# Kernel optimization log

Hardware: AMD Instinct MI355X
Metric: run time of the kernel (lower is better)

The kernel has to match this reference:

```python
import jax, jax.numpy as jnp
import numpy as np

N_NODES = 50000
IN_DIM = 256
OUT_DIM = 128
NUM_HEADS = 2
N_EDGES = 800000


def setup_inputs() -> dict:
    key = jax.random.key(0)
    k1, k2, k3, k4, k5 = jax.random.split(key, 5)
    x = jax.random.normal(k1, (N_NODES, IN_DIM), dtype=jnp.float32)
    edge_index = jax.random.randint(k2, (2, N_EDGES), 0, N_NODES, dtype=jnp.int64)
    # Linear(in_dim, out_dim*num_heads): store weight as [in_dim, out_dim*num_heads]
    fan = IN_DIM + OUT_DIM * NUM_HEADS
    W_w = jax.random.uniform(k3, (IN_DIM, OUT_DIM * NUM_HEADS), dtype=jnp.float32,
                             minval=-np.sqrt(6.0 / fan), maxval=np.sqrt(6.0 / fan))
    W_b = jnp.zeros((OUT_DIM * NUM_HEADS,), dtype=jnp.float32)
    # attention vector a: [2*out_dim], xavier uniform over (1, 2*out_dim)
    fa = 1 + 2 * OUT_DIM
    a = jax.random.uniform(k4, (2 * OUT_DIM,), dtype=jnp.float32,
                           minval=-np.sqrt(6.0 / fa), maxval=np.sqrt(6.0 / fa))
    return {"x": x, "edge_index": edge_index, "W_w": W_w, "W_b": W_b, "a": a}


def _gat_forward(x, edge_index, W_w, W_b, a):
    N = x.shape[0]
    H, D = NUM_HEADS, OUT_DIM
    Wh = (x @ W_w + W_b).reshape(N, H, D)  # [N, H, D]
    src, dst = edge_index[0], edge_index[1]
    a_src, a_dst = a[:D], a[D:]
    # per-node partial scores, then gather -> avoids [E, 2D] concat
    s = jnp.einsum('nhd,d->nh', Wh, a_src)  # [N, H]
    t = jnp.einsum('nhd,d->nh', Wh, a_dst)  # [N, H]
    e = jax.nn.leaky_relu(s[src] + t[dst], negative_slope=0.2)  # [E, H]
    # segment softmax over edges grouped by src node
    m = jax.ops.segment_max(e, src, num_segments=N)  # [N, H], -inf for empty
    ex = jnp.exp(e - m[src])
    denom = jax.ops.segment_sum(ex, src, num_segments=N)  # [N, H]
    alpha = ex / denom[src]  # [E, H]
    # weighted aggregation of destination features into source nodes
    agg = jax.ops.segment_sum(alpha[:, :, None] * Wh[dst], src, num_segments=N)  # [N, H, D]
    deg = jax.ops.segment_sum(jnp.ones_like(src, dtype=Wh.dtype), src, num_segments=N)  # [N]
    h_prime = jnp.where(deg[:, None, None] > 0, agg, Wh)
    return h_prime.reshape(N, H * D)


def reference(x, edge_index, W_w, W_b, a):
    return _gat_forward(x, edge_index, W_w, W_b, a)
```

## Files before the change

### kernel.cpp

```cpp
#include <hip/hip_runtime.h>
#include <hip/hip_bf16.h>
#include <math.h>

#define N_NODES 50000
#define IN_DIM 256
#define OUT_DIM 128
#define NUM_HEADS 2
#define N_EDGES 800000
#define F (OUT_DIM*NUM_HEADS)
#define SCAN_B 1024
#define N_SB ((N_NODES + SCAN_B - 1) / SCAN_B)
#define LDSP 264
#define CAP 128
#define N_COPIES 8
#define NBLK_H (N_EDGES / 256)

typedef __bf16 bf16;
typedef __bf16 bf16x8 __attribute__((ext_vector_type(8)));
typedef float  f32x4  __attribute__((ext_vector_type(4)));
typedef unsigned short u16x8 __attribute__((ext_vector_type(8)));

__global__ void k_transpose(const float* __restrict__ W, bf16* __restrict__ Wt,
                            int* __restrict__ deg8) {
    int k = blockIdx.x;
    int n = threadIdx.x;
    Wt[(size_t)n*IN_DIM + k] = (bf16)W[(size_t)k*F + n];
    int id = blockIdx.x * F + threadIdx.x;
    for (int i = id; i < N_COPIES * N_NODES; i += IN_DIM * F)
        deg8[i] = 0;
}

__global__ __launch_bounds__(256) void k_hist(const int* __restrict__ src,
                                              int* __restrict__ deg8,
                                              unsigned char* __restrict__ rank,
                                              int* __restrict__ xcdtab) {
    unsigned xcc;
    asm volatile("s_getreg_b32 %0, hwreg(HW_REG_XCC_ID, 0, 4)" : "=s"(xcc));
    xcc &= (N_COPIES - 1);
    if (threadIdx.x == 0) xcdtab[blockIdx.x] = (int)xcc;
    int e = blockIdx.x * 256 + threadIdx.x;
    int s = src[e];
    int r = __hip_atomic_fetch_add(&deg8[(size_t)xcc * N_NODES + s], 1,
                                   __ATOMIC_RELAXED, __HIP_MEMORY_SCOPE_WORKGROUP);
    rank[e] = (unsigned char)r;
}

__global__ __launch_bounds__(256, 2) void k_gemm(const float* __restrict__ X,
                                              const bf16* __restrict__ Wt,
                                              const float* __restrict__ Wb,
                                              const float* __restrict__ Av,
                                              bf16* __restrict__ Wh,
                                              float* __restrict__ s_arr,
                                              float* __restrict__ t_arr) {
    __shared__ bf16 As[64 * LDSP];
    __shared__ float sS[2][64], sT[2][64];
    int t = threadIdx.x;
    int wave = t >> 6, lane = t & 63;
    int quad = lane >> 4, l16 = lane & 15;
    int row0 = blockIdx.x * 64;
    int col0 = wave * 64;
    int h = wave >> 1;

    int rr = t >> 5;
    int cc = (t & 31) * 8;
    f32x4 slo[8], shi[8];
    #pragma unroll
    for (int i = 0; i < 8; ++i) {
        int r = row0 + 8*i + rr;
        r = (r < N_NODES) ? r : (N_NODES - 1);
        const float* p = X + (size_t)r * IN_DIM + cc;
        slo[i] = *(const f32x4*)p;
        shi[i] = *(const f32x4*)(p + 4);
    }

    bf16x8 bfrag[4][8];
    #pragma unroll
    for (int ni = 0; ni < 4; ++ni)
        #pragma unroll
        for (int ks = 0; ks < 8; ++ks)
            bfrag[ni][ks] = *(const bf16x8*)(Wt + (size_t)(col0 + ni*16 + l16)*IN_DIM
                                                + ks*32 + quad*8);

    #pragma unroll
    for (int i = 0; i < 8; ++i) {
        bf16x8 pk;
        #pragma unroll
        for (int q = 0; q < 4; ++q) {
            pk[q]   = (bf16)slo[i][q];
            pk[q+4] = (bf16)shi[i][q];
        }
        *(bf16x8*)(As + (8*i + rr) * LDSP + cc) = pk;
    }
    if (t < 128) { sS[t >> 6][t & 63] = 0.f; sT[t >> 6][t & 63] = 0.f; }
    __syncthreads();

    f32x4 acc[4][4] = {};
    #pragma unroll
    for (int ks = 0; ks < 8; ++ks) {
        int kb = ks * 32;
        bf16x8 afrag[4];
        #pragma unroll
        for (int mi = 0; mi < 4; ++mi)
            afrag[mi] = *(const bf16x8*)(As + (mi*16 + l16)*LDSP + kb + quad*8);

        #pragma unroll
        for (int mi = 0; mi < 4; ++mi)
            #pragma unroll
            for (int ni = 0; ni < 4; ++ni)
                acc[mi][ni] = __builtin_amdgcn_mfma_f32_16x16x32_bf16(
                                  afrag[mi], bfrag[ni][ks], acc[mi][ni], 0, 0, 0);
    }

    float bias_l[4], as_l[4], at_l[4];
    #pragma unroll
    for (int ni = 0; ni < 4; ++ni) {
        int c = col0 + ni*16 + l16;
        int d = c & (OUT_DIM - 1);
        bias_l[ni] = Wb[c];
        as_l[ni]   = Av[d];
        at_l[ni]   = Av[OUT_DIM + d];
    }

    #pragma unroll
    for (int mi = 0; mi < 4; ++mi) {
        #pragma unroll
        for (int reg = 0; reg < 4; ++reg) {
            int rl = mi*16 + quad*4 + reg;
            float ps = 0.f, pt = 0.f;
            #pragma unroll
            for (int ni = 0; ni < 4; ++ni) {
                float val = acc[mi][ni][reg] + bias_l[ni];
                ps += val * as_l[ni];
                pt += val * at_l[ni];
            }
            #pragma unroll
            for (int m = 8; m >= 1; m >>= 1) {
                ps += __shfl_xor(ps, m);
                pt += __shfl_xor(pt, m);
            }
            if ((lane & 15) == 0) {
                atomicAdd(&sS[h][rl], ps);
                atomicAdd(&sT[h][rl], pt);
            }
        }
    }

    __syncthreads();
    #pragma unroll
    for (int mi = 0; mi < 4; ++mi)
        #pragma unroll
        for (int ni = 0; ni < 4; ++ni) {
            int ccc = col0 + ni*16 + l16;
            #pragma unroll
            for (int reg = 0; reg < 4; ++reg) {
                int rl = mi*16 + quad*4 + reg;
                As[rl*LDSP + ccc] = (bf16)(acc[mi][ni][reg] + bias_l[ni]);
            }
        }
    __syncthreads();

    #pragma unroll
    for (int i = 0; i < 8; ++i) {
        int idx = i * 2048 + t * 8;
        int row = idx >> 8;
        int ccw = idx & 255;
        bf16x8 v = *(const bf16x8*)(As + row*LDSP + ccw);
        int grow = row0 + row;
        if (grow < N_NODES)
            *(bf16x8*)(Wh + (size_t)grow*F + ccw) = v;
    }

    if (t < 128) {
        int hh = t >> 6, rl = t & 63;
        int n = row0 + rl;
        if (n < N_NODES) {
            s_arr[n*2 + hh] = sS[hh][rl];
            t_arr[n*2 + hh] = sT[hh][rl];
        }
    }
}

__global__ __launch_bounds__(SCAN_B) void k_scan_local(const int* __restrict__ deg8,
                                                       int* __restrict__ excl,
                                                       int* __restrict__ bsum,
                                                       unsigned short* __restrict__ prefix8) {
    __shared__ int lds[SCAN_B];
    int t = threadIdx.x;
    int i = blockIdx.x * SCAN_B + t;
    int v = 0;
    if (i < N_NODES) {
        u16x8 pf;
        int run = 0;
        #pragma unroll
        for (int c = 0; c < N_COPIES; ++c) {
            pf[c] = (unsigned short)run;
            run += deg8[(size_t)c * N_NODES + i];
        }
        v = run;
        *(u16x8*)(prefix8 + (size_t)i * 8) = pf;
    }
    lds[t] = v;
    __syncthreads();
    for (int off = 1; off < SCAN_B; off <<= 1) {
        int u = (t >= off) ? lds[t - off] : 0;
        __syncthreads();
        lds[t] += u;
        __syncthreads();
    }
    if (i < N_NODES) excl[i] = lds[t] - v;
    if (t == SCAN_B - 1) bsum[blockIdx.x] = lds[t];
}

__global__ __launch_bounds__(256) void k_scan_final(const int* __restrict__ excl,
                                                    const int* __restrict__ bsum,
                                                    int* __restrict__ row_start) {
    __shared__ int sboff[64];
    int t = threadIdx.x;
    if (t < 64) {
        int orig = (t < N_SB) ? bsum[t] : 0;
        int v = orig;
        #pragma unroll
        for (int off = 1; off < 64; off <<= 1) {
            int u = __shfl_up(v, off);
            if (t >= off) v += u;
        }
        sboff[t] = v - orig;
        if (t == 63 && blockIdx.x == 0) row_start[N_NODES] = v;
    }
    __syncthreads();
    int i = blockIdx.x * 256 + t;
    if (i < N_NODES)
        row_start[i] = excl[i] + sboff[i >> 10];
}

__global__ __launch_bounds__(256) void k_scatter(const int* __restrict__ src,
                                                 const int* __restrict__ dst,
                                                 const unsigned char* __restrict__ rank,
                                                 const unsigned short* __restrict__ prefix8,
                                                 const int* __restrict__ row_start,
                                                 const int* __restrict__ xcdtab,
                                                 int* __restrict__ sorted_dst) {
    int e = blockIdx.x * 256 + threadIdx.x;
    int c = xcdtab[blockIdx.x];
    int s = src[e];
    int pos = row_start[s] + (int)prefix8[(size_t)s * 8 + c] + (int)rank[e];
    sorted_dst[pos] = dst[e];
}

__global__ __launch_bounds__(256) void k_agg(const bf16* __restrict__ Wh,
                                             const float* __restrict__ s_arr,
                                             const float* __restrict__ t_arr,
                                             const int* __restrict__ row_start,
                                             const int* __restrict__ sdst,
                                             float* __restrict__ out) {
    __shared__ float sp0[4][CAP];
    __shared__ float sp1[4][CAP];
    __shared__ int   sd[4][CAP];
    int wave = threadIdx.x >> 6, lane = threadIdx.x & 63;
    int n = blockIdx.x * 4 + wave;
    int sub = lane >> 5, cl = lane & 31;
    int c = cl * 8, h = cl >> 4;
    int beg = row_start[n], end = row_start[n + 1];
    if (beg == end) {
        if (sub == 0) {
            bf16x8 wh = *(const bf16x8*)(Wh + (size_t)n*F + c);
            f32x4 o0, o1;
            #pragma unroll
            for (int i = 0; i < 4; ++i) { o0[i] = (float)wh[i]; o1[i] = (float)wh[4+i]; }
            *(f32x4*)(out + (size_t)n*F + c)     = o0;
            *(f32x4*)(out + (size_t)n*F + c + 4) = o1;
        }
        return;
    }
    float2 sv = ((const float2*)s_arr)[n];
    float sum0 = 0.f, sum1 = 0.f;
    float a[8] = {0,0,0,0,0,0,0,0};
    float bacc[8] = {0,0,0,0,0,0,0,0};
    const float* sph = h ? sp1[wave] : sp0[wave];

    for (int c0 = beg; c0 < end; c0 += CAP) {
        int cnt = min(CAP, end - c0);
        for (int j = lane; j < cnt; j += 64) {
            int d = sdst[c0 + j];
            float2 tv = ((const float2*)t_arr)[d];
            float e0 = sv.x + tv.x; e0 = (e0 >= 0.f) ? e0 : 0.2f * e0;
            float e1 = sv.y + tv.y; e1 = (e1 >= 0.f) ? e1 : 0.2f * e1;
            float p0 = __expf(e0), p1 = __expf(e1);
            sp0[wave][j] = p0;
            sp1[wave][j] = p1;
            sd[wave][j]  = d;
            sum0 += p0;
            sum1 += p1;
        }
        int j = 0;
        for (; j + 8 <= cnt; j += 8) {
            int j0 = j + sub, j1 = j + 2 + sub, j2 = j + 4 + sub, j3 = j + 6 + sub;
            int d0 = sd[wave][j0], d1 = sd[wave][j1];
            int d2 = sd[wave][j2], d3 = sd[wave][j3];
            float p0 = sph[j0], p1 = sph[j1], p2 = sph[j2], p3 = sph[j3];
            bf16x8 w0 = *(const bf16x8*)(Wh + (size_t)d0*F + c);
            bf16x8 w1 = *(const bf16x8*)(Wh + (size_t)d1*F + c);
            bf16x8 w2 = *(const bf16x8*)(Wh + (size_t)d2*F + c);
            bf16x8 w3 = *(const bf16x8*)(Wh + (size_t)d3*F + c);
            #pragma unroll
            for (int i = 0; i < 8; ++i) {
                a[i]    += p0 * (float)w0[i];
                bacc[i] += p1 * (float)w1[i];
                a[i]    += p2 * (float)w2[i];
                bacc[i] += p3 * (float)w3[i];
            }
        }
        for (; j < cnt; j += 2) {
            int jj = j + sub;
            int jc = (jj < cnt) ? jj : 0;
            float p = (jj < cnt) ? sph[jc] : 0.f;
            int d = sd[wave][jc];
            bf16x8 w = *(const bf16x8*)(Wh + (size_t)d*F + c);
            #pragma unroll
            for (int i = 0; i < 8; ++i) a[i] += p * (float)w[i];
        }
    }
    #pragma unroll
    for (int m = 32; m >= 1; m >>= 1) {
        sum0 += __shfl_xor(sum0, m);
        sum1 += __shfl_xor(sum1, m);
    }
    float inv = 1.f / (h ? sum1 : sum0);
    #pragma unroll
    for (int i = 0; i < 8; ++i) {
        a[i] += bacc[i];
        a[i] += __shfl_xor(a[i], 32);
    }
    if (sub == 0) {
        f32x4 o0, o1;
        #pragma unroll
        for (int i = 0; i < 4; ++i) { o0[i] = a[i] * inv; o1[i] = a[4+i] * inv; }
        *(f32x4*)(out + (size_t)n*F + c)     = o0;
        *(f32x4*)(out + (size_t)n*F + c + 4) = o1;
    }
}

extern "C" void kernel_launch(void* const* d_in, const int* in_sizes, int n_in,
                              void* d_out, int out_size, void* d_ws, size_t ws_size,
                              hipStream_t stream) {
    const float* x  = (const float*)d_in[0];
    const int*   ei = (const int*)d_in[1];
    const float* Ww = (const float*)d_in[2];
    const float* Wb = (const float*)d_in[3];
    const float* a  = (const float*)d_in[4];
    float* out = (float*)d_out;
    const int* src = ei;
    const int* dst = ei + N_EDGES;

    char* ws = (char*)d_ws;
    bf16*  Wh        = (bf16*)ws;   ws += (size_t)N_NODES * F * 2;
    bf16*  Wt        = (bf16*)ws;   ws += (size_t)IN_DIM * F * 2;
    float* s_arr     = (float*)ws;  ws += (size_t)N_NODES * 2 * 4;
    float* t_arr     = (float*)ws;  ws += (size_t)N_NODES * 2 * 4;
    int*   excl      = (int*)ws;    ws += (size_t)N_NODES * 4;
    int*   bsum      = (int*)ws;    ws += 64 * 4;
    int*   row_start = (int*)ws;    ws += (size_t)(N_NODES + 1) * 4 + 12;
    unsigned short* prefix8 = (unsigned short*)ws; ws += (size_t)N_NODES * 8 * 2;
    unsigned char*  rank    = (unsigned char*)ws;  ws += (size_t)N_EDGES + 16;
    int*   xcdtab    = (int*)ws;    ws += (size_t)NBLK_H * 4 + 12;
    int*   sdst      = (int*)ws;    ws += (size_t)N_EDGES * 4;

    int* deg8 = sdst;

    k_transpose<<<IN_DIM, F, 0, stream>>>(Ww, Wt, deg8);
    k_hist<<<NBLK_H, 256, 0, stream>>>(src, deg8, rank, xcdtab);
    k_gemm<<<(N_NODES + 63) / 64, 256, 0, stream>>>(x, Wt, Wb, a, Wh, s_arr, t_arr);
    k_scan_local<<<N_SB, SCAN_B, 0, stream>>>(deg8, excl, bsum, prefix8);
    k_scan_final<<<(N_NODES + 255) / 256, 256, 0, stream>>>(excl, bsum, row_start);
    k_scatter<<<NBLK_H, 256, 0, stream>>>(src, dst, rank, prefix8,
                                          row_start, xcdtab, sdst);
    k_agg<<<N_NODES / 4, 256, 0, stream>>>(Wh, s_arr, t_arr, row_start, sdst, out);
}
```

Baseline: 250.0 us.

## Fuse histogram into GEMM launch and fold scan-final into scatter and aggregation

Merges the edge histogram kernel into the GEMM kernel by interleaving block roles (four histogram blocks per GEMM block), so the atomic-heavy histogram overlaps with the compute-bound GEMM in one launch. It also removes the separate scan-final kernel and the row_start array. Scatter and aggregation now recompute the 64-entry block offsets locally from bsum. This removes two launches and one global pass, at the cost of redundant small scans in every block and mixed block roles inside the fused kernel. Histogram blocks still request the GEMM kernel's LDS allocation, which may limit how many run at once.

```diff
diff --git a/kernel.cpp b/kernel.cpp
--- a/kernel.cpp
+++ b/kernel.cpp
@@ -13,7 +13,9 @@
 #define LDSP 264
 #define CAP 128
 #define N_COPIES 8
+#define NBLK_G ((N_NODES + 63) / 64)
 #define NBLK_H (N_EDGES / 256)
+#define NBLK_FUSED 3910
 
 typedef __bf16 bf16;
 typedef __bf16 bf16x8 __attribute__((ext_vector_type(8)));
@@ -30,34 +32,42 @@
         deg8[i] = 0;
 }
 
-__global__ __launch_bounds__(256) void k_hist(const int* __restrict__ src,
-                                              int* __restrict__ deg8,
-                                              unsigned char* __restrict__ rank,
-                                              int* __restrict__ xcdtab) {
-    unsigned xcc;
-    asm volatile("s_getreg_b32 %0, hwreg(HW_REG_XCC_ID, 0, 4)" : "=s"(xcc));
-    xcc &= (N_COPIES - 1);
-    if (threadIdx.x == 0) xcdtab[blockIdx.x] = (int)xcc;
-    int e = blockIdx.x * 256 + threadIdx.x;
-    int s = src[e];
-    int r = __hip_atomic_fetch_add(&deg8[(size_t)xcc * N_NODES + s], 1,
-                                   __ATOMIC_RELAXED, __HIP_MEMORY_SCOPE_WORKGROUP);
-    rank[e] = (unsigned char)r;
-}
-
-__global__ __launch_bounds__(256, 2) void k_gemm(const float* __restrict__ X,
+__global__ __launch_bounds__(256, 2) void k_gemm_hist(
+                                              const float* __restrict__ X,
                                               const bf16* __restrict__ Wt,
                                               const float* __restrict__ Wb,
                                               const float* __restrict__ Av,
+                                              const int* __restrict__ src,
+                                              int* __restrict__ deg8,
+                                              unsigned char* __restrict__ rank,
+                                              int* __restrict__ xcdtab,
                                               bf16* __restrict__ Wh,
                                               float* __restrict__ s_arr,
                                               float* __restrict__ t_arr) {
     __shared__ bf16 As[64 * LDSP];
     __shared__ float sS[2][64], sT[2][64];
+    int b = blockIdx.x;
+    int q = b / 5, r5 = b % 5;
     int t = threadIdx.x;
+
+    if (r5 != 4) {
+        int hi = q * 4 + r5;
+        if (hi >= NBLK_H) return;
+        unsigned xcc;
+        asm volatile("s_getreg_b32 %0, hwreg(HW_REG_XCC_ID, 0, 4)" : "=s"(xcc));
+        xcc &= (N_COPIES - 1);
+        if (t == 0) xcdtab[hi] = (int)xcc;
+        int e = hi * 256 + t;
+        int s = src[e];
+        int rr = __hip_atomic_fetch_add(&deg8[(size_t)xcc * N_NODES + s], 1,
+                                        __ATOMIC_RELAXED, __HIP_MEMORY_SCOPE_WORKGROUP);
+        rank[e] = (unsigned char)rr;
+        return;
+    }
+
     int wave = t >> 6, lane = t & 63;
     int quad = lane >> 4, l16 = lane & 15;
-    int row0 = blockIdx.x * 64;
+    int row0 = q * 64;
     int col0 = wave * 64;
     int h = wave >> 1;
 
@@ -85,9 +95,9 @@
     for (int i = 0; i < 8; ++i) {
         bf16x8 pk;
         #pragma unroll
-        for (int q = 0; q < 4; ++q) {
-            pk[q]   = (bf16)slo[i][q];
-            pk[q+4] = (bf16)shi[i][q];
+        for (int qq = 0; qq < 4; ++qq) {
+            pk[qq]   = (bf16)slo[i][qq];
+            pk[qq+4] = (bf16)shi[i][qq];
         }
         *(bf16x8*)(As + (8*i + rr) * LDSP + cc) = pk;
     }
@@ -211,9 +221,14 @@
     if (t == SCAN_B - 1) bsum[blockIdx.x] = lds[t];
 }
 
-__global__ __launch_bounds__(256) void k_scan_final(const int* __restrict__ excl,
-                                                    const int* __restrict__ bsum,
-                                                    int* __restrict__ row_start) {
+__global__ __launch_bounds__(256) void k_scatter(const int* __restrict__ src,
+                                                 const int* __restrict__ dst,
+                                                 const unsigned char* __restrict__ rank,
+                                                 const unsigned short* __restrict__ prefix8,
+                                                 const int* __restrict__ excl,
+                                                 const int* __restrict__ bsum,
+                                                 const int* __restrict__ xcdtab,
+                                                 int* __restrict__ sorted_dst) {
     __shared__ int sboff[64];
     int t = threadIdx.x;
     if (t < 64) {
@@ -225,42 +240,45 @@
             if (t >= off) v += u;
         }
         sboff[t] = v - orig;
-        if (t == 63 && blockIdx.x == 0) row_start[N_NODES] = v;
-    }
-    __syncthreads();
-    int i = blockIdx.x * 256 + t;
-    if (i < N_NODES)
-        row_start[i] = excl[i] + sboff[i >> 10];
-}
-
-__global__ __launch_bounds__(256) void k_scatter(const int* __restrict__ src,
-                                                 const int* __restrict__ dst,
-                                                 const unsigned char* __restrict__ rank,
-                                                 const unsigned short* __restrict__ prefix8,
-                                                 const int* __restrict__ row_start,
-                                                 const int* __restrict__ xcdtab,
-                                                 int* __restrict__ sorted_dst) {
-    int e = blockIdx.x * 256 + threadIdx.x;
+    }
+    __syncthreads();
+    int e = blockIdx.x * 256 + t;
     int c = xcdtab[blockIdx.x];
     int s = src[e];
-    int pos = row_start[s] + (int)prefix8[(size_t)s * 8 + c] + (int)rank[e];
+    int pos = excl[s] + sboff[s >> 10] + (int)prefix8[(size_t)s * 8 + c] + (int)rank[e];
     sorted_dst[pos] = dst[e];
 }
 
 __global__ __launch_bounds__(256) void k_agg(const bf16* __restrict__ Wh,
                                              const float* __restrict__ s_arr,
                                              const float* __restrict__ t_arr,
-                                             const int* __restrict__ row_start,
+                                             const int* __restrict__ excl,
+                                             const int* __restrict__ bsum,
                                              const int* __restrict__ sdst,
                                              float* __restrict__ out) {
     __shared__ float sp0[4][CAP];
     __shared__ float sp1[4][CAP];
     __shared__ int   sd[4][CAP];
-    int wave = threadIdx.x >> 6, lane = threadIdx.x & 63;
+    __shared__ int   sboff[64];
+    int t = threadIdx.x;
+    if (t < 64) {
+        int orig = (t < N_SB) ? bsum[t] : 0;
+        int v = orig;
+        #pragma unroll
+        for (int off = 1; off < 64; off <<= 1) {
+            int u = __shfl_up(v, off);
+            if (t >= off) v += u;
+        }
+        sboff[t] = v - orig;
+    }
+    __syncthreads();
+
+    int wave = t >> 6, lane = t & 63;
     int n = blockIdx.x * 4 + wave;
     int sub = lane >> 5, cl = lane & 31;
     int c = cl * 8, h = cl >> 4;
-    int beg = row_start[n], end = row_start[n + 1];
+    int beg = excl[n] + sboff[n >> 10];
+    int end = (n + 1 < N_NODES) ? excl[n + 1] + sboff[(n + 1) >> 10] : N_EDGES;
     if (beg == end) {
         if (sub == 0) {
             bf16x8 wh = *(const bf16x8*)(Wh + (size_t)n*F + c);
@@ -359,7 +377,6 @@
     float* t_arr     = (float*)ws;  ws += (size_t)N_NODES * 2 * 4;
     int*   excl      = (int*)ws;    ws += (size_t)N_NODES * 4;
     int*   bsum      = (int*)ws;    ws += 64 * 4;
-    int*   row_start = (int*)ws;    ws += (size_t)(N_NODES + 1) * 4 + 12;
     unsigned short* prefix8 = (unsigned short*)ws; ws += (size_t)N_NODES * 8 * 2;
     unsigned char*  rank    = (unsigned char*)ws;  ws += (size_t)N_EDGES + 16;
     int*   xcdtab    = (int*)ws;    ws += (size_t)NBLK_H * 4 + 12;
@@ -368,11 +385,10 @@
     int* deg8 = sdst;
 
     k_transpose<<<IN_DIM, F, 0, stream>>>(Ww, Wt, deg8);
-    k_hist<<<NBLK_H, 256, 0, stream>>>(src, deg8, rank, xcdtab);
-    k_gemm<<<(N_NODES + 63) / 64, 256, 0, stream>>>(x, Wt, Wb, a, Wh, s_arr, t_arr);
+    k_gemm_hist<<<NBLK_FUSED, 256, 0, stream>>>(x, Wt, Wb, a, src, deg8, rank,
+                                                xcdtab, Wh, s_arr, t_arr);
     k_scan_local<<<N_SB, SCAN_B, 0, stream>>>(deg8, excl, bsum, prefix8);
-    k_scan_final<<<(N_NODES + 255) / 256, 256, 0, stream>>>(excl, bsum, row_start);
     k_scatter<<<NBLK_H, 256, 0, stream>>>(src, dst, rank, prefix8,
-                                          row_start, xcdtab, sdst);
-    k_agg<<<N_NODES / 4, 256, 0, stream>>>(Wh, s_arr, t_arr, row_start, sdst, out);
-}
+                                          excl, bsum, xcdtab, sdst);
+    k_agg<<<N_NODES / 4, 256, 0, stream>>>(Wh, s_arr, t_arr, excl, bsum, sdst, out);
+}
```

Result: faster. 224.3 us (-10.3%).
